# Kernel optimization log

Measured on AMD Instinct MI355X. Metric: run time of the kernel, lower is better.

Reference implementation:

```python
import jax, jax.numpy as jnp
import numpy as np

TAU = 2.0        # spikingjelly LIFNode default
V_TH = 1.0       # default v_threshold
V_RESET = 0.0    # default v_reset (hard reset)


def setup_inputs() -> dict:
    key = jax.random.key(0)
    k1, k2, k3 = jax.random.split(key, 3)
    T, B, N, Cin, Cout = 4, 8, 1024, 512, 512
    x = jax.random.normal(k1, (T, B, N, Cin), dtype=jnp.float32)
    # nn.Linear weights are [out, in]; kaiming-uniform-ish scale
    W1 = jax.random.normal(k2, (Cout, Cin), dtype=jnp.float32) / np.sqrt(Cin)
    W2 = jax.random.normal(k3, (Cout, Cout), dtype=jnp.float32) / np.sqrt(Cout)
    return {"x": x, "W1": W1, "W2": W2}


def _spike(v):
    # forward heaviside (ATan surrogate only matters for backward)
    return (v >= V_TH).astype(v.dtype)


def _lif_multistep(h):
    # h: [T, B, N, C]; multi-step LIF with decay_input=True, hard reset to 0
    v0 = jnp.zeros(h.shape[1:], dtype=h.dtype)

    def step(v, x_t):
        v = v + (x_t - (v - V_RESET)) / TAU   # leaky integration
        s = _spike(v)                          # threshold
        v = v * (1.0 - s) + V_RESET * s        # hard reset
        return v, s

    _, spikes = jax.lax.scan(step, v0, h)
    return spikes  # [T, B, N, C]


def reference(x, W1, W2):
    h = jnp.einsum('tbni,oi->tbno', x, W1)      # Linear(in_ch, out_ch, bias=False)
    s = _lif_multistep(h)                        # LIFNode, step_mode='m'
    out = jnp.einsum('tbno,po->tbnp', s, W2)    # Linear(out_ch, out_ch, bias=False)
    return out.astype(jnp.float32)
```

## Files before the change

kernel.cpp:

```cpp
#include <hip/hip_runtime.h>


typedef _Float16 half8  __attribute__((ext_vector_type(8)));
typedef _Float16 half4v __attribute__((ext_vector_type(4)));
typedef float    f32x4  __attribute__((ext_vector_type(4)));

constexpr int TT   = 4;
constexpr int BB   = 8;
constexpr int NN   = 1024;
constexpr int CC   = 512;
constexpr int MROW = BB * NN;
constexpr int MTOT = TT * MROW;
constexpr int BNC  = MROW * CC;
constexpr int LDK  = 40;
constexpr int LTS2 = 132;

__global__ __launch_bounds__(256)
void gemm1_chain2(const float* __restrict__ X, const float* __restrict__ W,
                  float* __restrict__ H) {
#pragma clang fp contract(off)
    __shared__ float At[32][LTS2];
    __shared__ float Bt[32][LTS2];

    const int tid = threadIdx.x;
    const int RM  = blockIdx.x * 128;
    const int CN  = blockIdx.y * 128;
    const int tx  = tid & 15;
    const int ty  = tid >> 4;

    float acc[8][8] = {};

    for (int k0 = 0; k0 < CC; k0 += 32) {
        __syncthreads();
#pragma unroll
        for (int j = 0; j < 4; ++j) {
            int id  = tid + 256 * j;
            int row = id >> 3;
            int c4  = (id & 7) * 4;
            f32x4 va = *(const f32x4*)&X[(size_t)(RM + row) * CC + k0 + c4];
            f32x4 vb = *(const f32x4*)&W[(size_t)(CN + row) * CC + k0 + c4];
#pragma unroll
            for (int e = 0; e < 4; ++e) {
                At[c4 + e][row] = va[e];
                Bt[c4 + e][row] = vb[e];
            }
        }
        __syncthreads();

#pragma unroll 4
        for (int k = 0; k < 32; ++k) {
            f32x4 a0 = *(const f32x4*)&At[k][ty * 8];
            f32x4 a1 = *(const f32x4*)&At[k][ty * 8 + 4];
            f32x4 b0 = *(const f32x4*)&Bt[k][tx * 8];
            f32x4 b1 = *(const f32x4*)&Bt[k][tx * 8 + 4];
            float a[8] = {a0[0], a0[1], a0[2], a0[3], a1[0], a1[1], a1[2], a1[3]};
            float b[8] = {b0[0], b0[1], b0[2], b0[3], b1[0], b1[1], b1[2], b1[3]};
#pragma unroll
            for (int i = 0; i < 8; ++i)
#pragma unroll
                for (int jj = 0; jj < 8; ++jj)
                    acc[i][jj] = __builtin_fmaf(a[i], b[jj], acc[i][jj]);
        }
    }

#pragma unroll
    for (int i = 0; i < 8; ++i) {
        f32x4 o0 = {acc[i][0], acc[i][1], acc[i][2], acc[i][3]};
        f32x4 o1 = {acc[i][4], acc[i][5], acc[i][6], acc[i][7]};
        size_t base = (size_t)(RM + ty * 8 + i) * CC + CN + tx * 8;
        *(f32x4*)&H[base]     = o0;
        *(f32x4*)&H[base + 4] = o1;
    }
}

__global__ __launch_bounds__(256)
void lif_np(const float* __restrict__ H, _Float16* __restrict__ S) {
#pragma clang fp contract(off)
    int g = blockIdx.x * 256 + threadIdx.x;
    float v[4] = {0.f, 0.f, 0.f, 0.f};
#pragma unroll
    for (int t = 0; t < TT; ++t) {
        f32x4 h = *(const f32x4*)&H[(size_t)t * BNC + (size_t)g * 4];
        half4v s;
#pragma unroll
        for (int e = 0; e < 4; ++e) {
            float d  = h[e] - v[e];
            float d2 = d * 0.5f;
            v[e] = v[e] + d2;
            bool sp = v[e] >= 1.0f;
            s[e] = sp ? (_Float16)1.0f : (_Float16)0.0f;
            if (sp) v[e] = 0.0f;
        }
        *(half4v*)&S[(size_t)t * BNC + (size_t)g * 4] = s;
    }
}

__global__ __launch_bounds__(256)
void gemm2_f16(const _Float16* __restrict__ S, const float* __restrict__ W,
               float* __restrict__ O) {
    __shared__ _Float16 As[128][LDK], Bs[128][LDK];

    const int tid  = threadIdx.x;
    const int RM   = blockIdx.x * 128;
    const int CN   = blockIdx.y * 128;
    const int lane = tid & 63;
    const int wv   = tid >> 6;
    const int wr   = (wv >> 1) * 64;
    const int wc   = (wv & 1) * 64;
    const int r15  = lane & 15;
    const int kg   = lane >> 4;

    f32x4 acc[4][4] = {};

    for (int k0 = 0; k0 < CC; k0 += 32) {
        __syncthreads();
#pragma unroll
        for (int j = 0; j < 2; ++j) {
            int id  = tid + 256 * j;
            int row = id >> 2;
            int c8  = (id & 3) * 8;
            *(half8*)&As[row][c8] =
                *(const half8*)&S[(size_t)(RM + row) * CC + k0 + c8];
        }
#pragma unroll
        for (int j = 0; j < 4; ++j) {
            int id  = tid + 256 * j;
            int row = id >> 3;
            int c4  = (id & 7) * 4;
            f32x4 v = *(const f32x4*)&W[(size_t)(CN + row) * CC + k0 + c4];
            half4v hv;
#pragma unroll
            for (int e = 0; e < 4; ++e) hv[e] = (_Float16)v[e];
            *(half4v*)&Bs[row][c4] = hv;
        }
        __syncthreads();

        half8 a[4], b[4];
#pragma unroll
        for (int i = 0; i < 4; ++i) {
            a[i] = *(const half8*)&As[wr + i * 16 + r15][kg * 8];
            b[i] = *(const half8*)&Bs[wc + i * 16 + r15][kg * 8];
        }
#pragma unroll
        for (int i = 0; i < 4; ++i)
#pragma unroll
            for (int j = 0; j < 4; ++j)
                acc[i][j] = __builtin_amdgcn_mfma_f32_16x16x32_f16(a[i], b[j], acc[i][j], 0, 0, 0);
    }

#pragma unroll
    for (int i = 0; i < 4; ++i)
#pragma unroll
        for (int j = 0; j < 4; ++j)
#pragma unroll
            for (int r = 0; r < 4; ++r) {
                int gm = RM + wr + i * 16 + kg * 4 + r;
                int gn = CN + wc + j * 16 + r15;
                O[(size_t)gm * CC + gn] = acc[i][j][r];
            }
}

extern "C" void kernel_launch(void* const* d_in, const int* in_sizes, int n_in,
                              void* d_out, int out_size, void* d_ws, size_t ws_size,
                              hipStream_t stream) {
    const float* x  = (const float*)d_in[0];
    const float* W1 = (const float*)d_in[1];
    const float* W2 = (const float*)d_in[2];
    float* out = (float*)d_out;

    float*    h = out;
    _Float16* s = (_Float16*)d_ws;

    dim3 g1(MTOT / 128, CC / 128);
    gemm1_chain2<<<g1, 256, 0, stream>>>(x, W1, h);

    lif_np<<<BNC / 4 / 256, 256, 0, stream>>>(h, s);

    dim3 g2(MTOT / 128, CC / 128);
    gemm2_f16<<<g2, 256, 0, stream>>>(s, W2, out);
}
```

Before: 279.4 us.

## Widen FP32 GEMM1 tile to 128x256 with padded, rotated LDS layout

The first FP32 GEMM now computes a 128x256 output tile per block, so each thread holds an 8x16 accumulator and the A tile is loaded from global memory half as often. The transposed LDS tiles gain 4 floats of padding every 32 rows, and the scatter order of each thread's stores is rotated to cut bank conflicts. In exchange each thread needs far more registers (128 accumulators), which lowers occupancy and may cause spills, and the grid has half as many blocks.

```diff
diff --git a/kernel.cpp b/kernel.cpp
--- a/kernel.cpp
+++ b/kernel.cpp
@@ -13,22 +13,28 @@
 constexpr int MTOT = TT * MROW;
 constexpr int BNC  = MROW * CC;
 constexpr int LDK  = 40;
-constexpr int LTS2 = 132;
+constexpr int LTA  = 140;
+constexpr int LTB  = 284;
+
+__device__ __forceinline__ int PADI(int r) { return r + ((r >> 5) << 2); }
 
 __global__ __launch_bounds__(256)
-void gemm1_chain2(const float* __restrict__ X, const float* __restrict__ W,
+void gemm1_chain3(const float* __restrict__ X, const float* __restrict__ W,
                   float* __restrict__ H) {
 #pragma clang fp contract(off)
-    __shared__ float At[32][LTS2];
-    __shared__ float Bt[32][LTS2];
+    __shared__ float At[32][LTA];
+    __shared__ float Bt[32][LTB];
 
     const int tid = threadIdx.x;
     const int RM  = blockIdx.x * 128;
-    const int CN  = blockIdx.y * 128;
+    const int CN  = blockIdx.y * 256;
     const int tx  = tid & 15;
     const int ty  = tid >> 4;
-
-    float acc[8][8] = {};
+    const int abase = PADI(ty * 8);
+    const int bbase = PADI(tx * 16);
+    const int rot   = tid & 3;
+
+    float acc[8][16] = {};
 
     for (int k0 = 0; k0 < CC; k0 += 32) {
         __syncthreads();
@@ -37,39 +43,57 @@
             int id  = tid + 256 * j;
             int row = id >> 3;
             int c4  = (id & 7) * 4;
-            f32x4 va = *(const f32x4*)&X[(size_t)(RM + row) * CC + k0 + c4];
-            f32x4 vb = *(const f32x4*)&W[(size_t)(CN + row) * CC + k0 + c4];
+            f32x4 v = *(const f32x4*)&X[(size_t)(RM + row) * CC + k0 + c4];
+            int pr  = PADI(row);
 #pragma unroll
             for (int e = 0; e < 4; ++e) {
-                At[c4 + e][row] = va[e];
-                Bt[c4 + e][row] = vb[e];
+                int ee = (e + rot) & 3;
+                At[c4 + ee][pr] = v[ee];
             }
         }
-        __syncthreads();
-
-#pragma unroll 4
+#pragma unroll
+        for (int j = 0; j < 8; ++j) {
+            int id  = tid + 256 * j;
+            int row = id >> 3;
+            int c4  = (id & 7) * 4;
+            f32x4 v = *(const f32x4*)&W[(size_t)(CN + row) * CC + k0 + c4];
+            int pr  = PADI(row);
+#pragma unroll
+            for (int e = 0; e < 4; ++e) {
+                int ee = (e + rot) & 3;
+                Bt[c4 + ee][pr] = v[ee];
+            }
+        }
+        __syncthreads();
+
+#pragma unroll 2
         for (int k = 0; k < 32; ++k) {
-            f32x4 a0 = *(const f32x4*)&At[k][ty * 8];
-            f32x4 a1 = *(const f32x4*)&At[k][ty * 8 + 4];
-            f32x4 b0 = *(const f32x4*)&Bt[k][tx * 8];
-            f32x4 b1 = *(const f32x4*)&Bt[k][tx * 8 + 4];
-            float a[8] = {a0[0], a0[1], a0[2], a0[3], a1[0], a1[1], a1[2], a1[3]};
-            float b[8] = {b0[0], b0[1], b0[2], b0[3], b1[0], b1[1], b1[2], b1[3]};
+            f32x4 a0 = *(const f32x4*)&At[k][abase];
+            f32x4 a1 = *(const f32x4*)&At[k][abase + 4];
+            f32x4 b0 = *(const f32x4*)&Bt[k][bbase];
+            f32x4 b1 = *(const f32x4*)&Bt[k][bbase + 4];
+            f32x4 b2 = *(const f32x4*)&Bt[k][bbase + 8];
+            f32x4 b3 = *(const f32x4*)&Bt[k][bbase + 12];
+            float a[8]  = {a0[0], a0[1], a0[2], a0[3], a1[0], a1[1], a1[2], a1[3]};
+            float b[16] = {b0[0], b0[1], b0[2], b0[3], b1[0], b1[1], b1[2], b1[3],
+                           b2[0], b2[1], b2[2], b2[3], b3[0], b3[1], b3[2], b3[3]};
 #pragma unroll
             for (int i = 0; i < 8; ++i)
 #pragma unroll
-                for (int jj = 0; jj < 8; ++jj)
+                for (int jj = 0; jj < 16; ++jj)
                     acc[i][jj] = __builtin_fmaf(a[i], b[jj], acc[i][jj]);
         }
     }
 
 #pragma unroll
     for (int i = 0; i < 8; ++i) {
-        f32x4 o0 = {acc[i][0], acc[i][1], acc[i][2], acc[i][3]};
-        f32x4 o1 = {acc[i][4], acc[i][5], acc[i][6], acc[i][7]};
-        size_t base = (size_t)(RM + ty * 8 + i) * CC + CN + tx * 8;
-        *(f32x4*)&H[base]     = o0;
-        *(f32x4*)&H[base + 4] = o1;
+        size_t base = (size_t)(RM + ty * 8 + i) * CC + CN + tx * 16;
+#pragma unroll
+        for (int q = 0; q < 4; ++q) {
+            f32x4 o = {acc[i][q * 4], acc[i][q * 4 + 1],
+                       acc[i][q * 4 + 2], acc[i][q * 4 + 3]};
+            *(f32x4*)&H[base + q * 4] = o;
+        }
     }
 }
 
@@ -171,8 +195,8 @@
     float*    h = out;
     _Float16* s = (_Float16*)d_ws;
 
-    dim3 g1(MTOT / 128, CC / 128);
-    gemm1_chain2<<<g1, 256, 0, stream>>>(x, W1, h);
+    dim3 g1(MTOT / 128, CC / 256);
+    gemm1_chain3<<<g1, 256, 0, stream>>>(x, W1, h);
 
     lif_np<<<BNC / 4 / 256, 256, 0, stream>>>(h, s);
 
```

Result: faster. 271.1 us (-3.0%).
